# Performance work log

Measured on AMD Instinct MI355X. Metric: run time of the kernel, lower is better.

Reference implementation:

```python
import jax, jax.numpy as jnp
import numpy as np

B, N, E, F, G = 32, 512, 4, 128, 64
EMB, HID = 128, 256  # NodeEmbedding: Linear(E*G=256 -> 256) + BN + ELU + Linear(256 -> 128)
NUM_EDGES = 8192
BN_EPS = 1e-5


def setup_inputs() -> dict:
    key = jax.random.key(0)
    ks = jax.random.split(key, 8)
    X = jax.random.normal(ks[0], (B, N, F), dtype=jnp.float32)
    edges = jax.random.randint(ks[1], (B, E, 2, NUM_EDGES), 0, N, dtype=jnp.int64)
    # per-edge-type projection W_e: [F, G] (glorot)
    Ws = jax.random.normal(ks[2], (E, F, G), dtype=jnp.float32) * np.sqrt(2.0 / (F + G))
    # attention vectors a_e: [2G, 1]
    a = jax.random.normal(ks[3], (E, 2 * G, 1), dtype=jnp.float32) * (1.414 * np.sqrt(2.0 / (2 * G + 1)))
    lin0_w = jax.random.normal(ks[4], (E * G, HID), dtype=jnp.float32) * np.sqrt(2.0 / (E * G + HID))
    lin0_b = jnp.zeros((HID,), dtype=jnp.float32)
    bn_gamma = jnp.ones((HID,), dtype=jnp.float32)
    bn_beta = jnp.zeros((HID,), dtype=jnp.float32)
    lin1_w = jax.random.normal(ks[5], (HID, EMB), dtype=jnp.float32) * np.sqrt(2.0 / (HID + EMB))
    lin1_b = jnp.zeros((EMB,), dtype=jnp.float32)
    return {"X": X, "edges": edges, "Ws": Ws, "a": a, "lin0_w": lin0_w,
            "lin0_b": lin0_b, "bn_gamma": bn_gamma, "bn_beta": bn_beta,
            "lin1_w": lin1_w, "lin1_b": lin1_b}


def _dense_adj(edges):
    # COO -> dense, summing duplicates like torch.sparse_coo_tensor(...).to_dense()
    b_ix = jnp.arange(B)[:, None, None]
    e_ix = jnp.arange(E)[None, :, None]
    src = edges[:, :, 0, :]
    dst = edges[:, :, 1, :]
    A = jnp.zeros((B, E, N, N), dtype=jnp.float32)
    return A.at[b_ix, e_ix, src, dst].add(1.0)


def reference(X, edges, Ws, a, lin0_w, lin0_b, bn_gamma, bn_beta, lin1_w, lin1_b):
    A = _dense_adj(edges)                                   # [B,E,N,N]
    Wh = jnp.einsum('bnf,efg->beng', X, Ws)                 # [B,E,N,G]
    Wh1 = jnp.einsum('beng,ego->beno', Wh, a[:, :G, :])     # [B,E,N,1]
    Wh2 = jnp.einsum('beng,ego->beno', Wh, a[:, G:, :])     # [B,E,N,1]
    scores = (Wh1 + jnp.swapaxes(Wh2, 2, 3)) * A            # [B,E,N,N] (masked-to-0, NOT -inf: faithful)
    att = jax.nn.softmax(scores, axis=-1)
    H = jnp.einsum('benm,bemg->beng', att * A, Wh)          # [B,E,N,G]
    H = jnp.transpose(H, (0, 2, 1, 3)).reshape(B * N, E * G)
    # NodeEmbedding MLP (BatchNorm1d in training mode: batch stats, biased var)
    h = H @ lin0_w + lin0_b
    mu = jnp.mean(h, axis=0)
    var = jnp.mean((h - mu) ** 2, axis=0)
    h = (h - mu) * jax.lax.rsqrt(var + BN_EPS) * bn_gamma + bn_beta
    h = jax.nn.elu(h)
    out = h @ lin1_w + lin1_b
    return out.reshape(B, N, EMB)
```

## Files before the change

### kernel.cpp

```cpp
#include <hip/hip_runtime.h>

#define Bx 32
#define Nx 512
#define Ex 4
#define Fx 128
#define Gx 64
#define HIDx 256
#define EMBx 128
#define NEDGE 8192

typedef __attribute__((ext_vector_type(8))) short bf16x8;
typedef __attribute__((ext_vector_type(4))) float f32x4;

#define L2E 1.44269504f

__device__ __forceinline__ ushort f2bf(float x) {
    unsigned int u = __float_as_uint(x);
    u += 0x7fffu + ((u >> 16) & 1u);
    return (ushort)(u >> 16);
}
__device__ __forceinline__ float bf2f(ushort h) {
    return __uint_as_float(((unsigned int)h) << 16);
}

__global__ __launch_bounds__(256) void k0_convert(const float* __restrict__ w0,
                                                  const float* __restrict__ w1f,
                                                  const float* __restrict__ Wsf,
                                                  ushort* __restrict__ W0T,
                                                  ushort* __restrict__ W1T,
                                                  ushort* __restrict__ WsT) {
    int j = blockIdx.x, k = threadIdx.x;
    if (j < HIDx) {
        W0T[j * HIDx + k] = f2bf(w0[k * HIDx + j]);
    } else if (j < HIDx + EMBx) {
        int jj = j - HIDx;
        W1T[jj * HIDx + k] = f2bf(w1f[k * EMBx + jj]);
    } else {
        int eg = j - (HIDx + EMBx);
        if (k < Fx) {
            int e = eg >> 6, g = eg & 63;
            WsT[eg * Fx + k] = f2bf(Wsf[(e * Fx + k) * Gx + g]);
        }
    }
}

__global__ __launch_bounds__(256) void k1_wh(const float* __restrict__ X,
                                             const ushort* __restrict__ WsT,
                                             const float* __restrict__ a,
                                             ushort* __restrict__ Whb,
                                             float* __restrict__ w1,
                                             float* __restrict__ w2) {
    __shared__ ushort sXb[64 * 128];
    int id = blockIdx.x;
    int e = id & 3;
    int rest = id >> 2;
    int tile = rest & 7;
    int b = rest >> 3;
    int be = b * 4 + e;
    int n0 = tile * 64;
    int tid = threadIdx.x;
    for (int i = tid; i < 2048; i += 256) {
        int row = i >> 5, kq = i & 31;
        float4 xv = *(const float4*)&X[(size_t)(b * Nx + n0 + row) * Fx + kq * 4];
        ushort4 hv;
        hv.x = f2bf(xv.x); hv.y = f2bf(xv.y); hv.z = f2bf(xv.z); hv.w = f2bf(xv.w);
        unsigned int byteo = ((unsigned int)(row * 256 + kq * 8)) ^ (((unsigned int)(row & 7)) << 4);
        *(ushort4*)((char*)sXb + byteo) = hv;
    }
    __syncthreads();
    int wave = tid >> 6, lane = tid & 63;
    int arow = lane & 15, kg = lane >> 4;
    int row = wave * 16 + arow;
    f32x4 acc[4];
    #pragma unroll
    for (int t = 0; t < 4; ++t) acc[t] = (f32x4){0.f, 0.f, 0.f, 0.f};
    const ushort* WT = WsT + e * Gx * Fx;
    unsigned int aswz = ((unsigned int)(row & 7)) << 4;
    #pragma unroll
    for (int ks = 0; ks < 4; ++ks) {
        unsigned int abyte = ((unsigned int)(row * 256 + ks * 64 + kg * 16)) ^ aswz;
        bf16x8 af = *(const bf16x8*)((const char*)sXb + abyte);
        #pragma unroll
        for (int jt = 0; jt < 4; ++jt) {
            bf16x8 bf = *(const bf16x8*)&WT[(size_t)(jt * 16 + arow) * Fx + ks * 32 + kg * 8];
            acc[jt] = __builtin_amdgcn_mfma_f32_16x16x32_bf16(af, bf, acc[jt], 0, 0, 0);
        }
    }
    float a1v[4], a2v[4];
    #pragma unroll
    for (int jt = 0; jt < 4; ++jt) {
        a1v[jt] = a[e * 2 * Gx + jt * 16 + arow];
        a2v[jt] = a[e * 2 * Gx + Gx + jt * 16 + arow];
    }
    int m0 = n0 + wave * 16 + kg * 4;
    #pragma unroll
    for (int jt = 0; jt < 4; ++jt) {
        int g = jt * 16 + arow;
        ushort4 v;
        v.x = f2bf(acc[jt][0]); v.y = f2bf(acc[jt][1]);
        v.z = f2bf(acc[jt][2]); v.w = f2bf(acc[jt][3]);
        *(ushort4*)&Whb[((size_t)be * Gx + g) * Nx + m0] = v;
    }
    #pragma unroll
    for (int reg = 0; reg < 4; ++reg) {
        float p1 = acc[0][reg] * a1v[0] + acc[1][reg] * a1v[1] + acc[2][reg] * a1v[2] + acc[3][reg] * a1v[3];
        float p2 = acc[0][reg] * a2v[0] + acc[1][reg] * a2v[1] + acc[2][reg] * a2v[2] + acc[3][reg] * a2v[3];
        #pragma unroll
        for (int off = 1; off < 16; off <<= 1) {
            p1 += __shfl_xor(p1, off, 64);
            p2 += __shfl_xor(p2, off, 64);
        }
        if (arow == 0) {
            w1[be * Nx + m0 + reg] = p1;
            w2[be * Nx + m0 + reg] = p2;
        }
    }
}

__global__ __launch_bounds__(512) void k2_att(const int* __restrict__ edges,
                                              const ushort* __restrict__ Whb,
                                              const float* __restrict__ w1g,
                                              const float* __restrict__ w2g,
                                              ushort* __restrict__ Hb) {
    __shared__ ushort P[32 * 512];
    __shared__ float sw2s[512];
    __shared__ float sw1[32];
    __shared__ float sinv[32];
    unsigned int* cnt = (unsigned int*)P;
    int be = blockIdx.x; int b = be >> 2; int e = be & 3;
    int n0 = blockIdx.y * 32;
    int tid = threadIdx.x;
    for (int i = tid; i < 32 * 132; i += 512) cnt[i] = 0u;
    sw2s[tid ^ (((tid >> 5) & 7) << 2)] = w2g[be * Nx + tid] * L2E;
    if (tid < 32) sw1[tid] = w1g[be * Nx + n0 + tid] * L2E;
    __syncthreads();
    const int4* srcp = (const int4*)(edges + (size_t)be * 2 * NEDGE);
    const int4* dstp = (const int4*)(edges + (size_t)be * 2 * NEDGE + NEDGE);
    for (int i = tid; i < NEDGE / 4; i += 512) {
        int4 s4 = srcp[i]; int4 d4 = dstp[i];
        int ss[4] = {s4.x, s4.y, s4.z, s4.w};
        int dd[4] = {d4.x, d4.y, d4.z, d4.w};
        #pragma unroll
        for (int u = 0; u < 4; ++u) {
            unsigned int r = (unsigned int)(ss[u] - n0);
            if (r < 32u) atomicAdd(&cnt[r * 132 + (dd[u] >> 2)], 1u << ((dd[u] & 3) * 8));
        }
    }
    __syncthreads();
    int r = tid >> 4, c = tid & 15;
    unsigned int cw[8];
    const unsigned int* crow = cnt + r * 132 + c * 8;
    #pragma unroll
    for (int i = 0; i < 8; ++i) cw[i] = crow[i];
    float w1v = sw1[r];
    __syncthreads();
    float dsum = 0.f; int K = 0;
    #pragma unroll
    for (int tp = 0; tp < 4; ++tp) {
        unsigned int pkw[4];
        #pragma unroll
        for (int h = 0; h < 2; ++h) {
            unsigned int w = cw[tp * 2 + h];
            unsigned int nzm = (w | ((w & 0x7f7f7f7fu) + 0x7f7f7f7fu)) & 0x80808080u;
            K += __popc(nzm);
            int m0 = c * 32 + (tp * 2 + h) * 4;
            float4 s2 = *(const float4*)&sw2s[m0 ^ ((c & 7) << 2)];
            float sv[4] = {s2.x, s2.y, s2.z, s2.w};
            unsigned int lo = 0, hi = 0;
            #pragma unroll
            for (int jj = 0; jj < 4; ++jj) {
                unsigned int ccu = (w >> (jj * 8)) & 255u;
                float cf = (float)ccu;
                float ew = __builtin_exp2f(fminf((w1v + sv[jj]) * cf, 120.f));
                dsum += ccu ? ew : 0.f;
                unsigned int pb = (unsigned int)f2bf(ew * cf);
                if (jj & 2) hi |= pb << ((jj & 1) * 16);
                else        lo |= pb << ((jj & 1) * 16);
            }
            pkw[h * 2] = lo; pkw[h * 2 + 1] = hi;
        }
        uint4 pk = {pkw[0], pkw[1], pkw[2], pkw[3]};
        unsigned int byteo = ((unsigned int)(r * 1024 + c * 64 + tp * 16)) ^ (((unsigned int)(r & 7)) << 4);
        *(uint4*)((char*)P + byteo) = pk;
    }
    #pragma unroll
    for (int off = 1; off < 16; off <<= 1) {
        dsum += __shfl_xor(dsum, off, 64);
        K += __shfl_xor(K, off, 64);
    }
    if (c == 0) sinv[r] = 1.f / (dsum + (float)(Nx - K));
    __syncthreads();
    int wave = tid >> 6, lane = tid & 63;
    int wr = wave >> 2, wc = wave & 3;
    int row = wr * 16 + (lane & 15);
    int kgrp = lane >> 4;
    f32x4 acc = {0.f, 0.f, 0.f, 0.f};
    const ushort* WB = Whb + (size_t)be * Gx * Nx;
    int g0 = wc * 16 + (lane & 15);
    const ushort* Bp = WB + (size_t)g0 * Nx + kgrp * 8;
    unsigned int aswz = ((unsigned int)(row & 7)) << 4;
    __builtin_amdgcn_s_setprio(1);
    #pragma unroll
    for (int ks = 0; ks < 16; ++ks) {
        unsigned int abyte = ((unsigned int)(row * 1024 + ks * 64 + kgrp * 16)) ^ aswz;
        bf16x8 af = *(const bf16x8*)((const char*)P + abyte);
        bf16x8 bfv = *(const bf16x8*)(Bp + ks * 32);
        acc = __builtin_amdgcn_mfma_f32_16x16x32_bf16(af, bfv, acc, 0, 0, 0);
    }
    __builtin_amdgcn_s_setprio(0);
    float4 iv = *(const float4*)&sinv[wr * 16 + kgrp * 4];
    float ivv[4] = {iv.x, iv.y, iv.z, iv.w};
    #pragma unroll
    for (int reg = 0; reg < 4; ++reg) {
        int rr = n0 + wr * 16 + kgrp * 4 + reg;
        Hb[((size_t)(b * Nx) + rr) * (Ex * Gx) + e * Gx + wc * 16 + (lane & 15)] =
            f2bf(acc[reg] * ivv[reg]);
    }
}

__global__ __launch_bounds__(256) void k3_lin0(const ushort* __restrict__ Hb,
                                               const ushort* __restrict__ W0T,
                                               const float* __restrict__ lin0_b,
                                               ushort* __restrict__ h_pre,
                                               float* __restrict__ partials) {
    __shared__ float red_s[2][256], red_q[2][256];
    int tid = threadIdx.x, wave = tid >> 6, lane = tid & 63;
    int wr = wave >> 1, wc = wave & 1;
    int row0 = blockIdx.x * 32 + wr * 16;
    int arow = lane & 15, kg = lane >> 4;
    const ushort* A = Hb + (size_t)(row0 + arow) * HIDx;
    f32x4 acc[8];
    #pragma unroll
    for (int t = 0; t < 8; ++t) acc[t] = (f32x4){0.f, 0.f, 0.f, 0.f};
    #pragma unroll
    for (int ks = 0; ks < 8; ++ks) {
        int k0 = ks * 32 + kg * 8;
        bf16x8 af = *(const bf16x8*)&A[k0];
        #pragma unroll
        for (int jt = 0; jt < 8; ++jt) {
            bf16x8 bf = *(const bf16x8*)&W0T[(size_t)(wc * 128 + jt * 16 + arow) * HIDx + k0];
            acc[jt] = __builtin_amdgcn_mfma_f32_16x16x32_bf16(af, bf, acc[jt], 0, 0, 0);
        }
    }
    #pragma unroll
    for (int jt = 0; jt < 8; ++jt) {
        int col = wc * 128 + jt * 16 + arow;
        float b = lin0_b[col];
        float s = 0.f, q = 0.f;
        #pragma unroll
        for (int reg = 0; reg < 4; ++reg) {
            float v = acc[jt][reg] + b;
            h_pre[(size_t)(row0 + kg * 4 + reg) * HIDx + col] = f2bf(v);
            s += v; q += v * v;
        }
        s += __shfl_xor(s, 16, 64); s += __shfl_xor(s, 32, 64);
        q += __shfl_xor(q, 16, 64); q += __shfl_xor(q, 32, 64);
        if (lane < 16) { red_s[wr][col] = s; red_q[wr][col] = q; }
    }
    __syncthreads();
    int j = tid;
    partials[(size_t)blockIdx.x * 2 * HIDx + j] = red_s[0][j] + red_s[1][j];
    partials[(size_t)blockIdx.x * 2 * HIDx + HIDx + j] = red_q[0][j] + red_q[1][j];
}

__global__ __launch_bounds__(256) void k3b_stats(const float* __restrict__ partials,
                                                 const float* __restrict__ gamma,
                                                 const float* __restrict__ beta,
                                                 float* __restrict__ sb) {
    __shared__ float rs[8][32], rq[8][32];
    int jl = threadIdx.x & 31, sl = threadIdx.x >> 5;
    int j = blockIdx.x * 32 + jl;
    float s = 0.f, q = 0.f;
    for (int blk = sl; blk < 512; blk += 8) {
        s += partials[blk * 512 + j];
        q += partials[blk * 512 + 256 + j];
    }
    rs[sl][jl] = s; rq[sl][jl] = q;
    __syncthreads();
    if (threadIdx.x < 32) {
        float S = 0.f, Q = 0.f;
        #pragma unroll
        for (int t = 0; t < 8; ++t) { S += rs[t][jl]; Q += rq[t][jl]; }
        const float invM = 1.f / 16384.f;
        float mu = S * invM;
        float var = fmaxf(Q * invM - mu * mu, 0.f);
        float sc = gamma[j] * rsqrtf(var + 1e-5f);
        sb[j] = sc;
        sb[256 + j] = beta[j] - mu * sc;
    }
}

__global__ __launch_bounds__(256) void k4_lin1(const ushort* __restrict__ h_pre,
                                               const float* __restrict__ sb,
                                               const ushort* __restrict__ W1T,
                                               const float* __restrict__ lin1_b,
                                               float* __restrict__ out) {
    int tid = threadIdx.x, wave = tid >> 6, lane = tid & 63;
    int wr = wave >> 1, wc = wave & 1;
    int row0 = blockIdx.x * 32 + wr * 16;
    int arow = lane & 15, kg = lane >> 4;
    const ushort* A = h_pre + (size_t)(row0 + arow) * HIDx;
    f32x4 acc[4];
    #pragma unroll
    for (int t = 0; t < 4; ++t) acc[t] = (f32x4){0.f, 0.f, 0.f, 0.f};
    #pragma unroll
    for (int ks = 0; ks < 8; ++ks) {
        int k0 = ks * 32 + kg * 8;
        bf16x8 hv = *(const bf16x8*)&A[k0];
        float4 sc0 = *(const float4*)&sb[k0];
        float4 sc1 = *(const float4*)&sb[k0 + 4];
        float4 bi0 = *(const float4*)&sb[256 + k0];
        float4 bi1 = *(const float4*)&sb[256 + k0 + 4];
        float scv[8] = {sc0.x, sc0.y, sc0.z, sc0.w, sc1.x, sc1.y, sc1.z, sc1.w};
        float biv[8] = {bi0.x, bi0.y, bi0.z, bi0.w, bi1.x, bi1.y, bi1.z, bi1.w};
        bf16x8 af;
        #pragma unroll
        for (int u = 0; u < 8; ++u) {
            float v = bf2f((ushort)hv[u]) * scv[u] + biv[u];
            v = v > 0.f ? v : expm1f(v);
            af[u] = (short)f2bf(v);
        }
        #pragma unroll
        for (int jt = 0; jt < 4; ++jt) {
            bf16x8 bf = *(const bf16x8*)&W1T[(size_t)(wc * 64 + jt * 16 + arow) * HIDx + k0];
            acc[jt] = __builtin_amdgcn_mfma_f32_16x16x32_bf16(af, bf, acc[jt], 0, 0, 0);
        }
    }
    #pragma unroll
    for (int jt = 0; jt < 4; ++jt) {
        int col = wc * 64 + jt * 16 + arow;
        float b = lin1_b[col];
        #pragma unroll
        for (int reg = 0; reg < 4; ++reg)
            out[(size_t)(row0 + kg * 4 + reg) * EMBx + col] = acc[jt][reg] + b;
    }
}

extern "C" void kernel_launch(void* const* d_in, const int* in_sizes, int n_in,
                              void* d_out, int out_size, void* d_ws, size_t ws_size,
                              hipStream_t stream) {
    const float* X      = (const float*)d_in[0];
    const int*   edges  = (const int*)d_in[1];
    const float* Ws     = (const float*)d_in[2];
    const float* a      = (const float*)d_in[3];
    const float* lin0_w = (const float*)d_in[4];
    const float* lin0_b = (const float*)d_in[5];
    const float* gamma  = (const float*)d_in[6];
    const float* beta   = (const float*)d_in[7];
    const float* lin1_w = (const float*)d_in[8];
    const float* lin1_b = (const float*)d_in[9];
    float* ws = (float*)d_ws;

    ushort* Whb     = (ushort*)ws;
    ushort* h_pre   = (ushort*)ws;
    ushort* Hb      = (ushort*)(ws + 4194304);
    float*  w1      = ws + 8388608;
    float*  w2      = ws + 8454144;
    float*  partials= ws + 8519680;
    float*  sb      = ws + 8781824;
    ushort* WsT     = (ushort*)(ws + 8782336);
    ushort* W0T     = (ushort*)(ws + 8798720);
    ushort* W1T     = (ushort*)(ws + 8831488);
    float*  out     = (float*)d_out;

    k0_convert<<<dim3(HIDx + EMBx + 256), 256, 0, stream>>>(lin0_w, lin1_w, Ws, W0T, W1T, WsT);
    k1_wh  <<<dim3(1024), 256, 0, stream>>>(X, WsT, a, Whb, w1, w2);
    k2_att <<<dim3(Bx * Ex, Nx / 32), 512, 0, stream>>>(edges, Whb, w1, w2, Hb);
    k3_lin0<<<dim3(512), 256, 0, stream>>>(Hb, W0T, lin0_b, h_pre, partials);
    k3b_stats<<<8, 256, 0, stream>>>(partials, gamma, beta, sb);
    k4_lin1<<<dim3(512), 256, 0, stream>>>(h_pre, sb, W1T, lin1_b, out);
}
```

Measured before the change: 130.5 us.

## Pre-bin edges by source tile and compute attention weights only for nonzeros

The weight-conversion kernel now also counting-sorts each (batch, edge-type) edge list by 32-row source tile, packing each edge into a ushort and writing per-tile offsets. The attention kernel then reads only the edges for its own tile, instead of scanning all 8192 edges in every one of the 16 tile blocks. The probability tile is zero-filled first, and exp is computed and stored only for nonzero adjacency counts, skipping the dense exp over mostly empty rows. The costs are an extra binning pass with LDS atomics and divergent scalar LDS stores in place of packed vector stores.

```diff
diff --git a/kernel.cpp b/kernel.cpp
--- a/kernel.cpp
+++ b/kernel.cpp
@@ -23,24 +23,72 @@
     return __uint_as_float(((unsigned int)h) << 16);
 }
 
-__global__ __launch_bounds__(256) void k0_convert(const float* __restrict__ w0,
-                                                  const float* __restrict__ w1f,
-                                                  const float* __restrict__ Wsf,
-                                                  ushort* __restrict__ W0T,
-                                                  ushort* __restrict__ W1T,
-                                                  ushort* __restrict__ WsT) {
-    int j = blockIdx.x, k = threadIdx.x;
-    if (j < HIDx) {
+__global__ __launch_bounds__(512) void k0b(const int* __restrict__ edges,
+                                           const float* __restrict__ w0,
+                                           const float* __restrict__ w1f,
+                                           const float* __restrict__ Wsf,
+                                           ushort* __restrict__ W0T,
+                                           ushort* __restrict__ W1T,
+                                           ushort* __restrict__ WsT,
+                                           ushort* __restrict__ binned,
+                                           int* __restrict__ offs) {
+    __shared__ int hist8[8][16];
+    __shared__ int offl[17];
+    __shared__ int cur[16];
+    int blk = blockIdx.x, tid = threadIdx.x;
+    if (blk < 128) {
+        int wave = tid >> 6;
+        for (int i = tid; i < 128; i += 512) ((int*)hist8)[i] = 0;
+        __syncthreads();
+        const int4* s4p = (const int4*)(edges + (size_t)blk * 2 * NEDGE);
+        const int4* d4p = (const int4*)(edges + (size_t)blk * 2 * NEDGE + NEDGE);
+        for (int i = tid; i < NEDGE / 4; i += 512) {
+            int4 s4 = s4p[i];
+            atomicAdd(&hist8[wave][s4.x >> 5], 1);
+            atomicAdd(&hist8[wave][s4.y >> 5], 1);
+            atomicAdd(&hist8[wave][s4.z >> 5], 1);
+            atomicAdd(&hist8[wave][s4.w >> 5], 1);
+        }
+        __syncthreads();
+        if (tid == 0) {
+            int run = 0;
+            for (int t = 0; t < 16; ++t) {
+                offl[t] = run;
+                int s = 0;
+                #pragma unroll
+                for (int w = 0; w < 8; ++w) s += hist8[w][t];
+                run += s;
+            }
+            offl[16] = run;
+            for (int t = 0; t <= 16; ++t) offs[blk * 17 + t] = offl[t];
+        }
+        __syncthreads();
+        if (tid < 16) cur[tid] = offl[tid];
+        __syncthreads();
+        ushort* bout = binned + (size_t)blk * NEDGE;
+        for (int i = tid; i < NEDGE / 4; i += 512) {
+            int4 s4 = s4p[i]; int4 d4 = d4p[i];
+            int ss[4] = {s4.x, s4.y, s4.z, s4.w};
+            int dd[4] = {d4.x, d4.y, d4.z, d4.w};
+            #pragma unroll
+            for (int u = 0; u < 4; ++u) {
+                int t = ss[u] >> 5;
+                int pos = atomicAdd(&cur[t], 1);
+                bout[pos] = (ushort)(((ss[u] & 31) << 9) | dd[u]);
+            }
+        }
+    } else if (blk < 256) {
+        int idx = (blk - 128) * 512 + tid;
+        int j = idx >> 8, k = idx & 255;
         W0T[j * HIDx + k] = f2bf(w0[k * HIDx + j]);
-    } else if (j < HIDx + EMBx) {
-        int jj = j - HIDx;
-        W1T[jj * HIDx + k] = f2bf(w1f[k * EMBx + jj]);
+    } else if (blk < 320) {
+        int idx = (blk - 256) * 512 + tid;
+        int j = idx >> 8, k = idx & 255;
+        W1T[j * HIDx + k] = f2bf(w1f[k * EMBx + j]);
     } else {
-        int eg = j - (HIDx + EMBx);
-        if (k < Fx) {
-            int e = eg >> 6, g = eg & 63;
-            WsT[eg * Fx + k] = f2bf(Wsf[(e * Fx + k) * Gx + g]);
-        }
+        int idx = (blk - 320) * 512 + tid;
+        int eg = idx >> 7, f = idx & 127;
+        WsT[eg * Fx + f] = f2bf(Wsf[((eg >> 6) * Fx + f) * Gx + (eg & 63)]);
     }
 }
 
@@ -117,34 +165,29 @@
     }
 }
 
-__global__ __launch_bounds__(512) void k2_att(const int* __restrict__ edges,
+__global__ __launch_bounds__(512) void k2_att(const ushort* __restrict__ binned,
+                                              const int* __restrict__ offs,
                                               const ushort* __restrict__ Whb,
                                               const float* __restrict__ w1g,
                                               const float* __restrict__ w2g,
                                               ushort* __restrict__ Hb) {
     __shared__ ushort P[32 * 512];
-    __shared__ float sw2s[512];
+    __shared__ float sw2[512];
     __shared__ float sw1[32];
     __shared__ float sinv[32];
     unsigned int* cnt = (unsigned int*)P;
     int be = blockIdx.x; int b = be >> 2; int e = be & 3;
-    int n0 = blockIdx.y * 32;
+    int tile = blockIdx.y; int n0 = tile * 32;
     int tid = threadIdx.x;
     for (int i = tid; i < 32 * 132; i += 512) cnt[i] = 0u;
-    sw2s[tid ^ (((tid >> 5) & 7) << 2)] = w2g[be * Nx + tid] * L2E;
+    sw2[tid] = w2g[be * Nx + tid] * L2E;
     if (tid < 32) sw1[tid] = w1g[be * Nx + n0 + tid] * L2E;
     __syncthreads();
-    const int4* srcp = (const int4*)(edges + (size_t)be * 2 * NEDGE);
-    const int4* dstp = (const int4*)(edges + (size_t)be * 2 * NEDGE + NEDGE);
-    for (int i = tid; i < NEDGE / 4; i += 512) {
-        int4 s4 = srcp[i]; int4 d4 = dstp[i];
-        int ss[4] = {s4.x, s4.y, s4.z, s4.w};
-        int dd[4] = {d4.x, d4.y, d4.z, d4.w};
-        #pragma unroll
-        for (int u = 0; u < 4; ++u) {
-            unsigned int r = (unsigned int)(ss[u] - n0);
-            if (r < 32u) atomicAdd(&cnt[r * 132 + (dd[u] >> 2)], 1u << ((dd[u] & 3) * 8));
-        }
+    int t0 = offs[be * 17 + tile], t1 = offs[be * 17 + tile + 1];
+    const ushort* bin = binned + (size_t)be * NEDGE;
+    for (int i = t0 + tid; i < t1; i += 512) {
+        unsigned int pk = bin[i];
+        atomicAdd(&cnt[(pk >> 9) * 132 + ((pk & 511u) >> 2)], 1u << ((pk & 3u) * 8));
     }
     __syncthreads();
     int r = tid >> 4, c = tid & 15;
@@ -154,34 +197,29 @@
     for (int i = 0; i < 8; ++i) cw[i] = crow[i];
     float w1v = sw1[r];
     __syncthreads();
+    unsigned int swz = ((unsigned int)(r & 7)) << 4;
+    unsigned int rowb = (unsigned int)(r * 1024);
+    #pragma unroll
+    for (int tp = 0; tp < 4; ++tp) {
+        uint4 z = {0u, 0u, 0u, 0u};
+        *(uint4*)((char*)P + ((rowb + (unsigned int)(c * 64 + tp * 16)) ^ swz)) = z;
+    }
     float dsum = 0.f; int K = 0;
     #pragma unroll
-    for (int tp = 0; tp < 4; ++tp) {
-        unsigned int pkw[4];
-        #pragma unroll
-        for (int h = 0; h < 2; ++h) {
-            unsigned int w = cw[tp * 2 + h];
-            unsigned int nzm = (w | ((w & 0x7f7f7f7fu) + 0x7f7f7f7fu)) & 0x80808080u;
-            K += __popc(nzm);
-            int m0 = c * 32 + (tp * 2 + h) * 4;
-            float4 s2 = *(const float4*)&sw2s[m0 ^ ((c & 7) << 2)];
-            float sv[4] = {s2.x, s2.y, s2.z, s2.w};
-            unsigned int lo = 0, hi = 0;
-            #pragma unroll
-            for (int jj = 0; jj < 4; ++jj) {
-                unsigned int ccu = (w >> (jj * 8)) & 255u;
-                float cf = (float)ccu;
-                float ew = __builtin_exp2f(fminf((w1v + sv[jj]) * cf, 120.f));
-                dsum += ccu ? ew : 0.f;
-                unsigned int pb = (unsigned int)f2bf(ew * cf);
-                if (jj & 2) hi |= pb << ((jj & 1) * 16);
-                else        lo |= pb << ((jj & 1) * 16);
-            }
-            pkw[h * 2] = lo; pkw[h * 2 + 1] = hi;
-        }
-        uint4 pk = {pkw[0], pkw[1], pkw[2], pkw[3]};
-        unsigned int byteo = ((unsigned int)(r * 1024 + c * 64 + tp * 16)) ^ (((unsigned int)(r & 7)) << 4);
-        *(uint4*)((char*)P + byteo) = pk;
+    for (int t = 0; t < 8; ++t) {
+        unsigned int w = cw[t];
+        if (!w) continue;
+        int dbase = c * 32 + t * 4;
+        #pragma unroll
+        for (int jj = 0; jj < 4; ++jj) {
+            unsigned int ccu = (w >> (jj * 8)) & 255u;
+            if (!ccu) continue;
+            K++;
+            float cf = (float)ccu;
+            float ew = __builtin_exp2f(fminf((w1v + sw2[dbase + jj]) * cf, 120.f));
+            dsum += ew;
+            *(ushort*)((char*)P + ((rowb + (unsigned int)((dbase + jj) * 2)) ^ swz)) = f2bf(ew * cf);
+        }
     }
     #pragma unroll
     for (int off = 1; off < 16; off <<= 1) {
@@ -353,6 +391,8 @@
 
     ushort* Whb     = (ushort*)ws;
     ushort* h_pre   = (ushort*)ws;
+    ushort* binned  = (ushort*)ws + 4194304;
+    int*    offs    = (int*)(ws + 2621440);
     ushort* Hb      = (ushort*)(ws + 4194304);
     float*  w1      = ws + 8388608;
     float*  w2      = ws + 8454144;
@@ -363,9 +403,9 @@
     ushort* W1T     = (ushort*)(ws + 8831488);
     float*  out     = (float*)d_out;
 
-    k0_convert<<<dim3(HIDx + EMBx + 256), 256, 0, stream>>>(lin0_w, lin1_w, Ws, W0T, W1T, WsT);
+    k0b    <<<dim3(384), 512, 0, stream>>>(edges, lin0_w, lin1_w, Ws, W0T, W1T, WsT, binned, offs);
     k1_wh  <<<dim3(1024), 256, 0, stream>>>(X, WsT, a, Whb, w1, w2);
-    k2_att <<<dim3(Bx * Ex, Nx / 32), 512, 0, stream>>>(edges, Whb, w1, w2, Hb);
+    k2_att <<<dim3(Bx * Ex, Nx / 32), 512, 0, stream>>>(binned, offs, Whb, w1, w2, Hb);
     k3_lin0<<<dim3(512), 256, 0, stream>>>(Hb, W0T, lin0_b, h_pre, partials);
     k3b_stats<<<8, 256, 0, stream>>>(partials, gamma, beta, sb);
     k4_lin1<<<dim3(512), 256, 0, stream>>>(h_pre, sb, W1T, lin1_b, out);
```

After: 128.7 us. About the same (-1.4%).
